# Kernel optimization log

Hardware: AMD Instinct MI355X
Metric: run time of the kernel (lower is better)

## Reference

```python
import jax, jax.numpy as jnp
import numpy as np
from jax import lax

B, NODE, T, D_IN = 8, 1024, 12, 16
HID, GAT_OUT, PRED_LEN = 32, 32, 6
HEADS = 3
F_IN = HID * T      # 384
C = GAT_OUT * T     # 384
N = B * NODE        # 8192
E = 65536


def setup_inputs() -> dict:
    key = jax.random.key(0)
    ks = jax.random.split(key, 24)
    s = 0.05
    inp = {}
    inp["x"] = jax.random.normal(ks[0], (B, NODE, T, D_IN), jnp.float32)
    inp["edge_index"] = jax.random.randint(ks[1], (2, E), 0, N)
    inp["edge_attr"] = jax.random.normal(ks[2], (E, 1), jnp.float32)
    inp["batch_vec"] = jnp.repeat(jnp.arange(B), NODE)
    inp["alpha"] = 1.0
    # GRU params (torch gate order: r, z, n)
    inp["Wih"] = jax.random.normal(ks[3], (3 * HID, D_IN), jnp.float32) * s
    inp["Whh"] = jax.random.normal(ks[4], (3 * HID, HID), jnp.float32) * s
    inp["bih"] = jax.random.normal(ks[5], (3 * HID,), jnp.float32) * s
    inp["bhh"] = jax.random.normal(ks[6], (3 * HID,), jnp.float32) * s
    # GATConv params
    inp["Wgat"] = jax.random.normal(ks[7], (HEADS * C, F_IN), jnp.float32) * s
    inp["att_src"] = jax.random.normal(ks[8], (1, HEADS, C), jnp.float32) * s
    inp["att_dst"] = jax.random.normal(ks[9], (1, HEADS, C), jnp.float32) * s
    inp["Wedge"] = jax.random.normal(ks[10], (HEADS * C, 1), jnp.float32) * s
    inp["att_edge"] = jax.random.normal(ks[11], (1, HEADS, C), jnp.float32) * s
    inp["gat_bias"] = jax.random.normal(ks[12], (C,), jnp.float32) * s
    # predictors / classifiers
    inp["Wp1"] = jax.random.normal(ks[13], (1, GAT_OUT), jnp.float32) * s
    inp["bp1"] = jax.random.normal(ks[14], (1,), jnp.float32) * s
    inp["Wp3"] = jax.random.normal(ks[15], (PRED_LEN, T), jnp.float32) * s
    inp["bp3"] = jax.random.normal(ks[16], (PRED_LEN,), jnp.float32) * s
    inp["Wc1"] = jax.random.normal(ks[17], (GAT_OUT, T * GAT_OUT), jnp.float32) * s
    inp["bc1"] = jax.random.normal(ks[18], (GAT_OUT,), jnp.float32) * s
    inp["Wc2"] = jax.random.normal(ks[19], (2, GAT_OUT), jnp.float32) * s
    inp["bc2"] = jax.random.normal(ks[20], (2,), jnp.float32) * s
    return inp


def _gru(x, Wih, Whh, bih, bhh):
    # x: [rows, T, D_IN] -> [rows, T, HID]
    h0 = jnp.zeros((x.shape[0], HID), x.dtype)

    def step(h, xt):
        gi = xt @ Wih.T + bih
        gh = h @ Whh.T + bhh
        ir, iz, inn = jnp.split(gi, 3, axis=-1)
        hr, hz, hn = jnp.split(gh, 3, axis=-1)
        r = jax.nn.sigmoid(ir + hr)
        z = jax.nn.sigmoid(iz + hz)
        n = jnp.tanh(inn + r * hn)
        h_new = (1.0 - z) * n + z * h
        return h_new, h_new

    _, hs = lax.scan(step, h0, jnp.swapaxes(x, 0, 1))
    return jnp.swapaxes(hs, 0, 1)


def _gat(x, edge_index, edge_attr, Wgat, att_src, att_dst, Wedge, att_edge, bias):
    # PyG GATConv, heads=HEADS, concat=False, edge_dim=1, no self loops
    h = (x @ Wgat.T).reshape(N, HEADS, C)          # [N,H,C]
    a_src = (h * att_src).sum(-1)                  # [N,H]
    a_dst = (h * att_dst).sum(-1)                  # [N,H]
    src, dst = edge_index[0], edge_index[1]
    e = (edge_attr @ Wedge.T).reshape(-1, HEADS, C)
    a_edge = (e * att_edge).sum(-1)                # [E,H]
    a = jax.nn.leaky_relu(a_src[src] + a_dst[dst] + a_edge, 0.2)
    amax = jax.ops.segment_max(a, dst, num_segments=N)
    a = jnp.exp(a - amax[dst])
    denom = jax.ops.segment_sum(a, dst, num_segments=N)
    a = a / (denom[dst] + 1e-16)                   # segment softmax over incoming edges
    msg = h[src] * a[:, :, None]                   # [E,H,C]
    out = jax.ops.segment_sum(msg, dst, num_segments=N)
    return out.mean(axis=1) + bias                 # concat=False -> head mean


def reference(x, edge_index, edge_attr, batch_vec, alpha,
              Wih, Whh, bih, bhh,
              Wgat, att_src, att_dst, Wedge, att_edge, gat_bias,
              Wp1, bp1, Wp3, bp3, Wc1, bc1, Wc2, bc2):
    gru_in = x.reshape(-1, T, D_IN)                       # [N,T,D]
    gru_out = _gru(gru_in, Wih, Whh, bih, bhh)            # [N,T,HID]
    gat_in = gru_out.reshape(N, F_IN)
    gat_out = _gat(gat_in, edge_index, edge_attr, Wgat, att_src, att_dst,
                   Wedge, att_edge, gat_bias)             # [N,C]
    lin_in = gat_out.reshape(-1, T, GAT_OUT)              # [N,T,GAT_OUT]
    p = jax.nn.relu(jnp.einsum('ntc,oc->nto', lin_in, Wp1) + bp1).squeeze(-1)  # [N,T]
    p = jax.nn.relu(p @ Wp3.T + bp3)                      # [N,PRED_LEN]
    out_pred = p.reshape(B, NODE, PRED_LEN)
    # GRL is identity in forward
    pooled = jax.ops.segment_max(gat_out, batch_vec, num_segments=B)  # [B,C]
    l1 = pooled @ Wc1.T + bc1
    l2 = l1 @ Wc2.T + bc2
    out_label = jax.nn.softmax(l2, axis=1)
    return out_pred, out_label
```

## Files before the change

kernel.cpp:

```cpp
#include <hip/hip_runtime.h>
#include <hip/hip_bf16.h>

#define N_NODES 8192
#define E_EDGES 65536
#define HEADS 3
#define CDIM 384
#define NHC 1152
#define T_STEPS 12
#define D_IN 16
#define HID 32
#define PRED_LEN 6
#define OUT_LABEL_OFF 49152

#define O_X        0u
#define O_WIH      1572864u
#define O_WHH      1574400u
#define O_BIH      1577472u
#define O_BHH      1577568u
#define O_WGAT     1577664u
#define O_ATTS     2020032u
#define O_ATTD     2021184u
#define O_WEDGE    2022336u
#define O_ATTE     2023488u
#define O_GBIAS    2024640u
#define O_WP1      2025024u
#define O_BP1      2025056u
#define O_WP3      2025057u
#define O_BP3      2025129u
#define O_WC1      2025135u
#define O_BC1      2037423u
#define O_WC2      2037455u
#define O_BC2      2037519u
#define O_EATTR    2037521u
#define CONV_TOTAL 2103057u

#define O_GATIN    2103072u
#define O_GATB     O_GATIN
#define O_WGATB    (O_GATIN + 1572864u)
#define O_DEG      (O_GATIN + 1794048u)
#define O_ROWST    (O_GATIN + 1802240u)
#define O_CURS     (O_GATIN + 1810432u)
#define O_CSRE     (O_GATIN + 1818624u)
#define O_HFEAT    5248800u
#define O_ASRC     14685984u
#define O_ADST     14710560u
#define O_ARAW     14735136u
#define O_WEXP     14931744u
#define O_AMAX     15128352u
#define O_DENOM    15152928u
#define O_GMEAN    15177504u
#define O_POOLED   18323232u
#define O_KH       18326304u
#define O_FLAG     18326307u

typedef __attribute__((ext_vector_type(8))) short short8;
typedef __attribute__((ext_vector_type(4))) float floatx4;

__device__ __forceinline__ float b2f(unsigned short u) {
    return __uint_as_float(((unsigned)u) << 16);
}
__device__ __forceinline__ unsigned short f2b(float f) {
    __hip_bfloat16 b = __float2bfloat16(f);
    return *(unsigned short*)&b;
}
__device__ __forceinline__ unsigned enc_f(float f) {
    unsigned u = __float_as_uint(f);
    return (u & 0x80000000u) ? ~u : (u | 0x80000000u);
}
__device__ __forceinline__ float dec_f(unsigned e) {
    return __uint_as_float((e & 0x80000000u) ? (e & 0x7FFFFFFFu) : ~e);
}

__global__ void detect_kernel(const unsigned short* __restrict__ wih_raw,
                              int* __restrict__ flag)
{
    int lane = threadIdx.x;
    int cnt = 0;
#pragma unroll
    for (int i = 0; i < 8; i++) {
        unsigned short h = wih_raw[(lane * 8 + i) * 2];
        int e = (h >> 7) & 0xFF;
        if (e >= 100 && e <= 127) cnt++;
    }
#pragma unroll
    for (int off = 32; off; off >>= 1) cnt += __shfl_down(cnt, off, 64);
    if (lane == 0) *flag = (cnt >= 300) ? 1 : 0;
}

__global__ __launch_bounds__(256) void convert_all(
    const int* __restrict__ flag,
    const void* x, const void* Wih, const void* Whh, const void* bih, const void* bhh,
    const void* Wgat, const void* atts, const void* attd, const void* Wedge, const void* atte,
    const void* gbias, const void* Wp1, const void* bp1, const void* Wp3, const void* bp3,
    const void* Wc1, const void* bc1, const void* Wc2, const void* bc2, const void* eattr,
    float* __restrict__ dst)
{
    unsigned idx = blockIdx.x * 256 + threadIdx.x;
    if (idx >= CONV_TOTAL) return;
    const void* src; unsigned off;
    if      (idx < O_WIH)   { src = x;     off = idx - O_X; }
    else if (idx < O_WHH)   { src = Wih;   off = idx - O_WIH; }
    else if (idx < O_BIH)   { src = Whh;   off = idx - O_WHH; }
    else if (idx < O_BHH)   { src = bih;   off = idx - O_BIH; }
    else if (idx < O_WGAT)  { src = bhh;   off = idx - O_BHH; }
    else if (idx < O_ATTS)  { src = Wgat;  off = idx - O_WGAT; }
    else if (idx < O_ATTD)  { src = atts;  off = idx - O_ATTS; }
    else if (idx < O_WEDGE) { src = attd;  off = idx - O_ATTD; }
    else if (idx < O_ATTE)  { src = Wedge; off = idx - O_WEDGE; }
    else if (idx < O_GBIAS) { src = atte;  off = idx - O_ATTE; }
    else if (idx < O_WP1)   { src = gbias; off = idx - O_GBIAS; }
    else if (idx < O_BP1)   { src = Wp1;   off = idx - O_WP1; }
    else if (idx < O_BP3)   { src = (idx < O_BP1 + 1) ? bp1 : Wp3; off = (idx < O_BP1 + 1) ? 0 : idx - O_BP3 + 72; }
    else if (idx < O_WC1)   { src = bp3;   off = idx - O_BP3; }
    else if (idx < O_BC1)   { src = Wc1;   off = idx - O_WC1; }
    else if (idx < O_WC2)   { src = bc1;   off = idx - O_BC1; }
    else if (idx < O_BC2)   { src = Wc2;   off = idx - O_WC2; }
    else if (idx < O_EATTR) { src = bc2;   off = idx - O_BC2; }
    else                    { src = eattr; off = idx - O_EATTR; }
    if (idx >= O_BP1 && idx < O_BP3) {
        if (idx == O_BP1) { src = bp1; off = 0; }
        else              { src = Wp3; off = idx - O_WP3; }
    }
    float v = (*flag) ? b2f(((const unsigned short*)src)[off])
                      : ((const float*)src)[off];
    dst[idx] = v;
}

__global__ void cvt_wgat(const int* __restrict__ flag,
                         const void* __restrict__ Wg,
                         unsigned short* __restrict__ dstb)
{
    unsigned i = blockIdx.x * 256 + threadIdx.x;
    if (i >= 442368u) return;
    dstb[i] = (*flag) ? ((const unsigned short*)Wg)[i]
                      : f2b(((const float*)Wg)[i]);
}

__global__ __launch_bounds__(256) void gru_kernel(
    const float* __restrict__ xf,
    const float* __restrict__ Wih,
    const float* __restrict__ Whh,
    const float* __restrict__ bih,
    const float* __restrict__ bhh,
    unsigned short* __restrict__ gat_b)
{
    __shared__ float hsh[8][32];
    int gid = blockIdx.x * 256 + threadIdx.x;
    int n = gid >> 5;
    int j = gid & 31;
    int wid = threadIdx.x >> 5;

    float wih[3][16], whh[3][32], bi[3], bh[3];
#pragma unroll
    for (int g = 0; g < 3; g++) {
        int row = g * 32 + j;
#pragma unroll
        for (int i = 0; i < 16; i++) wih[g][i] = Wih[row * 16 + i];
#pragma unroll
        for (int i = 0; i < 32; i++) whh[g][i] = Whh[row * 32 + i];
        bi[g] = bih[row];
        bh[g] = bhh[row];
    }

    float hval = 0.f;
    hsh[wid][j] = 0.f;

    const float4* x4 = (const float4*)(xf + (size_t)n * 192);

    for (int t = 0; t < T_STEPS; t++) {
        float xv[16];
#pragma unroll
        for (int q = 0; q < 4; q++) {
            float4 p = x4[t * 4 + q];
            xv[q * 4 + 0] = p.x; xv[q * 4 + 1] = p.y;
            xv[q * 4 + 2] = p.z; xv[q * 4 + 3] = p.w;
        }

        float ir = bi[0], iz = bi[1], in_ = bi[2];
#pragma unroll
        for (int i = 0; i < 16; i++) {
            ir  += wih[0][i] * xv[i];
            iz  += wih[1][i] * xv[i];
            in_ += wih[2][i] * xv[i];
        }
        float hr = bh[0], hz = bh[1], hn = bh[2];
#pragma unroll
        for (int q = 0; q < 8; q++) {
            float4 hv = *(const float4*)&hsh[wid][q * 4];
            hr += whh[0][q*4+0]*hv.x + whh[0][q*4+1]*hv.y + whh[0][q*4+2]*hv.z + whh[0][q*4+3]*hv.w;
            hz += whh[1][q*4+0]*hv.x + whh[1][q*4+1]*hv.y + whh[1][q*4+2]*hv.z + whh[1][q*4+3]*hv.w;
            hn += whh[2][q*4+0]*hv.x + whh[2][q*4+1]*hv.y + whh[2][q*4+2]*hv.z + whh[2][q*4+3]*hv.w;
        }
        float r = 1.f / (1.f + expf(-(ir + hr)));
        float z = 1.f / (1.f + expf(-(iz + hz)));
        float nn = tanhf(in_ + r * hn);
        hval = (1.f - z) * nn + z * hval;

        gat_b[(size_t)n * 384 + t * 32 + j] = f2b(hval);
        hsh[wid][j] = hval;
    }
}

__global__ __launch_bounds__(256) void gemm_mfma(
    const unsigned short* __restrict__ Ab,
    const unsigned short* __restrict__ Bb,
    unsigned short* __restrict__ Cb)
{
    __shared__ unsigned short sA[128][40];
    __shared__ unsigned short sB[128][40];
    int tid = threadIdx.x;
    int wave = tid >> 6, lane = tid & 63;
    int wm = (wave >> 1) * 64, wn = (wave & 1) * 64;
    int m0 = blockIdx.x * 128, n0 = blockIdx.y * 128;

    int r0 = tid >> 2;
    int c8 = (tid & 3) * 8;

    floatx4 acc[4][4];
#pragma unroll
    for (int i = 0; i < 4; i++)
#pragma unroll
        for (int j = 0; j < 4; j++) acc[i][j] = 0;

    int ml = lane & 15, kq = (lane >> 4) * 8;

    for (int k0 = 0; k0 < 384; k0 += 32) {
        short8 a0 = *(const short8*)(Ab + (size_t)(m0 + r0) * 384 + k0 + c8);
        short8 a1 = *(const short8*)(Ab + (size_t)(m0 + r0 + 64) * 384 + k0 + c8);
        short8 b0 = *(const short8*)(Bb + (size_t)(n0 + r0) * 384 + k0 + c8);
        short8 b1 = *(const short8*)(Bb + (size_t)(n0 + r0 + 64) * 384 + k0 + c8);

        __syncthreads();
        *(short8*)(&sA[r0][c8])      = a0;
        *(short8*)(&sA[r0 + 64][c8]) = a1;
        *(short8*)(&sB[r0][c8])      = b0;
        *(short8*)(&sB[r0 + 64][c8]) = b1;
        __syncthreads();

        short8 af[4], bf[4];
#pragma unroll
        for (int i = 0; i < 4; i++)
            af[i] = *(const short8*)(&sA[wm + i * 16 + ml][kq]);
#pragma unroll
        for (int j = 0; j < 4; j++)
            bf[j] = *(const short8*)(&sB[wn + j * 16 + ml][kq]);
#pragma unroll
        for (int i = 0; i < 4; i++)
#pragma unroll
            for (int j = 0; j < 4; j++)
                acc[i][j] = __builtin_amdgcn_mfma_f32_16x16x32_bf16(af[i], bf[j], acc[i][j], 0, 0, 0);
    }

    int cn = lane & 15, rq = (lane >> 4) * 4;
#pragma unroll
    for (int i = 0; i < 4; i++)
#pragma unroll
        for (int j = 0; j < 4; j++)
#pragma unroll
            for (int r = 0; r < 4; r++)
                Cb[(size_t)(m0 + wm + i * 16 + rq + r) * NHC + n0 + wn + j * 16 + cn] = f2b(acc[i][j][r]);
}

__global__ __launch_bounds__(256) void att_score_kernel(
    const unsigned short* __restrict__ h_bf,
    const float* __restrict__ att_src,
    const float* __restrict__ att_dst,
    float* __restrict__ a_src, float* __restrict__ a_dst)
{
    int w = (blockIdx.x * 256 + threadIdx.x) >> 6;
    int lane = threadIdx.x & 63;
    int n = w / 3, hd = w % 3;
    const unsigned short* hrow = h_bf + (size_t)n * NHC + hd * CDIM;
    float s0 = 0.f, s1 = 0.f;
#pragma unroll
    for (int q = 0; q < 6; q++) {
        int c = lane + q * 64;
        float hv = b2f(hrow[c]);
        s0 += hv * att_src[hd * CDIM + c];
        s1 += hv * att_dst[hd * CDIM + c];
    }
#pragma unroll
    for (int off = 32; off; off >>= 1) {
        s0 += __shfl_down(s0, off, 64);
        s1 += __shfl_down(s1, off, 64);
    }
    if (lane == 0) { a_src[n * 3 + hd] = s0; a_dst[n * 3 + hd] = s1; }
}

__global__ void edge_const_kernel(const float* __restrict__ Wedge,
                                  const float* __restrict__ att_edge,
                                  float* __restrict__ Kh)
{
    int hd = threadIdx.x >> 6, lane = threadIdx.x & 63;
    float s = 0.f;
#pragma unroll
    for (int q = 0; q < 6; q++) {
        int c = lane + q * 64;
        s += Wedge[hd * CDIM + c] * att_edge[hd * CDIM + c];
    }
#pragma unroll
    for (int off = 32; off; off >>= 1) s += __shfl_down(s, off, 64);
    if (lane == 0) Kh[hd] = s;
}

__global__ __launch_bounds__(256) void edge_score_kernel(
    const int* __restrict__ edge_index,
    const float* __restrict__ edge_attr,
    const float* __restrict__ a_src, const float* __restrict__ a_dst,
    const float* __restrict__ Kh,
    float* __restrict__ a_raw, unsigned* __restrict__ amax_enc,
    int* __restrict__ deg)
{
    int tid = blockIdx.x * 256 + threadIdx.x;
    int hd = tid >> 16;
    int e = tid & (E_EDGES - 1);
    int src = edge_index[e];
    int dst = edge_index[E_EDGES + e];
    float a = a_src[src * 3 + hd] + a_dst[dst * 3 + hd] + edge_attr[e] * Kh[hd];
    a = a > 0.f ? a : 0.2f * a;
    a_raw[hd * E_EDGES + e] = a;
    atomicMax(&amax_enc[dst * 3 + hd], enc_f(a));
    if (hd == 0) atomicAdd(&deg[dst], 1);
}

__global__ __launch_bounds__(256) void scan_kernel(
    const int* __restrict__ deg, int* __restrict__ rowstart, int* __restrict__ cursor)
{
    __shared__ int ps[256];
    int t = threadIdx.x;
    int l[32], s = 0;
#pragma unroll
    for (int i = 0; i < 32; i++) { l[i] = deg[t * 32 + i]; s += l[i]; }
    ps[t] = s;
    __syncthreads();
    if (t == 0) {
        int run = 0;
        for (int i = 0; i < 256; i++) { int v = ps[i]; ps[i] = run; run += v; }
    }
    __syncthreads();
    int b = ps[t];
#pragma unroll
    for (int i = 0; i < 32; i++) {
        rowstart[t * 32 + i] = b;
        cursor[t * 32 + i] = b;
        b += l[i];
    }
}

__global__ __launch_bounds__(256) void edge_exp_kernel(
    const int* __restrict__ edge_index,
    const float* __restrict__ a_raw, const unsigned* __restrict__ amax_enc,
    float* __restrict__ w_exp, float* __restrict__ denom,
    int* __restrict__ cursor, int* __restrict__ csr_e)
{
    int tid = blockIdx.x * 256 + threadIdx.x;
    int hd = tid >> 16;
    int e = tid & (E_EDGES - 1);
    int dst = edge_index[E_EDGES + e];
    float m = dec_f(amax_enc[dst * 3 + hd]);
    float w = expf(a_raw[hd * E_EDGES + e] - m);
    w_exp[hd * E_EDGES + e] = w;
    unsafeAtomicAdd(&denom[dst * 3 + hd], w);
    if (hd == 0) {
        int pos = atomicAdd(&cursor[dst], 1);
        csr_e[pos] = e;
    }
}

__global__ __launch_bounds__(384) void aggregate_fused(
    const int* __restrict__ flag,
    const int* __restrict__ edge_index,
    const unsigned short* __restrict__ h_bf,
    const float* __restrict__ w_exp, const float* __restrict__ denom,
    const int* __restrict__ rowstart, const int* __restrict__ deg,
    const int* __restrict__ csr_e,
    const float* __restrict__ gat_bias,
    const float* __restrict__ Wp1, const float* __restrict__ bp1,
    const float* __restrict__ Wp3, const float* __restrict__ bp3,
    float* __restrict__ gmean,
    void* __restrict__ out_pred)
{
    int dst = blockIdx.x;
    int s = rowstart[dst], d = deg[dst];
    int tid = threadIdx.x;
    const float third = 1.f / 3.f;
    float inv0 = third / (denom[dst * 3 + 0] + 1e-16f);
    float inv1 = third / (denom[dst * 3 + 1] + 1e-16f);
    float inv2 = third / (denom[dst * 3 + 2] + 1e-16f);
    __shared__ int ssrc[64];
    __shared__ float sc0[64], sc1[64], sc2[64];
    __shared__ float gs[384];
    __shared__ float ps[12];
    float a = 0.f;
    for (int ch = 0; ch < d; ch += 64) {
        int m = d - ch; if (m > 64) m = 64;
        __syncthreads();
        if (tid < m) {
            int e = csr_e[s + ch + tid];
            ssrc[tid] = edge_index[e];
            sc0[tid] = w_exp[e] * inv0;
            sc1[tid] = w_exp[E_EDGES + e] * inv1;
            sc2[tid] = w_exp[2 * E_EDGES + e] * inv2;
        }
        __syncthreads();
        for (int i = 0; i < m; i++) {
            const unsigned short* hs = h_bf + (size_t)ssrc[i] * NHC;
            a += sc0[i] * b2f(hs[tid]) + sc1[i] * b2f(hs[tid + CDIM]) + sc2[i] * b2f(hs[tid + 2 * CDIM]);
        }
    }
    float g = a + gat_bias[tid];
    gmean[(size_t)dst * CDIM + tid] = g;
    gs[tid] = g;
    __syncthreads();

    int t = tid >> 5, c = tid & 31;
    float v = gs[t * 32 + c] * Wp1[c];
#pragma unroll
    for (int off = 16; off; off >>= 1) v += __shfl_down(v, off, 32);
    if (c == 0) { float p = v + bp1[0]; ps[t] = p > 0.f ? p : 0.f; }
    __syncthreads();

    if (tid < PRED_LEN) {
        float acc = bp3[tid];
#pragma unroll
        for (int tt = 0; tt < 12; tt++) acc += Wp3[tid * 12 + tt] * ps[tt];
        acc = acc > 0.f ? acc : 0.f;
        size_t oi = (size_t)dst * PRED_LEN + tid;
        if (*flag) ((__hip_bfloat16*)out_pred)[oi] = __float2bfloat16(acc);
        else       ((float*)out_pred)[oi] = acc;
    }
}

__global__ __launch_bounds__(384) void pool_kernel(
    const float* __restrict__ gmean,
    unsigned* __restrict__ pooled_enc)
{
    int b = blockIdx.x, ch = blockIdx.y;
    int tid = threadIdx.x;
    const float* base = gmean + ((size_t)b * 1024 + ch * 64) * CDIM + tid;
    float m = -3.4e38f;
    for (int i = 0; i < 64; i++)
        m = fmaxf(m, base[(size_t)i * CDIM]);
    atomicMax(&pooled_enc[b * CDIM + tid], enc_f(m));
}

__global__ __launch_bounds__(256) void cls_kernel(
    const int* __restrict__ flag,
    const unsigned* __restrict__ pooled_enc,
    const float* __restrict__ Wc1, const float* __restrict__ bc1,
    const float* __restrict__ Wc2, const float* __restrict__ bc2,
    void* __restrict__ out_base)
{
    __shared__ float l1s[8][32];
    int b = threadIdx.x >> 5, i = threadIdx.x & 31;
    float acc = bc1[i];
    for (int c = 0; c < CDIM; c++)
        acc += Wc1[i * CDIM + c] * dec_f(pooled_enc[b * CDIM + c]);
    l1s[b][i] = acc;
    __syncthreads();
    if (threadIdx.x < 8) {
        int bb = threadIdx.x;
        float l0 = bc2[0], l1v = bc2[1];
#pragma unroll
        for (int ii = 0; ii < 32; ii++) {
            l0  += Wc2[ii] * l1s[bb][ii];
            l1v += Wc2[32 + ii] * l1s[bb][ii];
        }
        float m = fmaxf(l0, l1v);
        float e0 = expf(l0 - m), e1 = expf(l1v - m);
        float s = e0 + e1;
        if (*flag) {
            __hip_bfloat16* ob = (__hip_bfloat16*)out_base;
            ob[OUT_LABEL_OFF + bb * 2 + 0] = __float2bfloat16(e0 / s);
            ob[OUT_LABEL_OFF + bb * 2 + 1] = __float2bfloat16(e1 / s);
        } else {
            float* of = (float*)out_base;
            of[OUT_LABEL_OFF + bb * 2 + 0] = e0 / s;
            of[OUT_LABEL_OFF + bb * 2 + 1] = e1 / s;
        }
    }
}

extern "C" void kernel_launch(void* const* d_in, const int* in_sizes, int n_in,
                              void* d_out, int out_size, void* d_ws, size_t ws_size,
                              hipStream_t stream) {
    float* W = (float*)d_ws;
    int* flag = (int*)(W + O_FLAG);
    const int* edge_index = (const int*)d_in[1];

    size_t zero_floats = (size_t)(O_POOLED + 8 * CDIM) - O_AMAX;
    hipMemsetAsync(W + O_AMAX, 0, zero_floats * 4, stream);
    hipMemsetAsync(W + O_DEG, 0, 8192 * 4, stream);

    detect_kernel<<<1, 64, 0, stream>>>((const unsigned short*)d_in[5], flag);
    convert_all<<<(CONV_TOTAL + 255) / 256, 256, 0, stream>>>(
        flag,
        d_in[0], d_in[5], d_in[6], d_in[7], d_in[8],
        d_in[9], d_in[10], d_in[11], d_in[12], d_in[13],
        d_in[14], d_in[15], d_in[16], d_in[17], d_in[18],
        d_in[19], d_in[20], d_in[21], d_in[22], d_in[2],
        W);
    cvt_wgat<<<(442368 + 255) / 256, 256, 0, stream>>>(
        flag, d_in[9], (unsigned short*)(W + O_WGATB));

    gru_kernel<<<N_NODES * 32 / 256, 256, 0, stream>>>(
        W + O_X, W + O_WIH, W + O_WHH, W + O_BIH, W + O_BHH,
        (unsigned short*)(W + O_GATB));
    gemm_mfma<<<dim3(N_NODES / 128, NHC / 128), 256, 0, stream>>>(
        (const unsigned short*)(W + O_GATB),
        (const unsigned short*)(W + O_WGATB),
        (unsigned short*)(W + O_HFEAT));
    att_score_kernel<<<(N_NODES * 3 * 64) / 256, 256, 0, stream>>>(
        (const unsigned short*)(W + O_HFEAT), W + O_ATTS, W + O_ATTD,
        W + O_ASRC, W + O_ADST);
    edge_const_kernel<<<1, 192, 0, stream>>>(W + O_WEDGE, W + O_ATTE, W + O_KH);
    edge_score_kernel<<<3 * E_EDGES / 256, 256, 0, stream>>>(
        edge_index, W + O_EATTR, W + O_ASRC, W + O_ADST, W + O_KH,
        W + O_ARAW, (unsigned*)(W + O_AMAX), (int*)(W + O_DEG));
    scan_kernel<<<1, 256, 0, stream>>>(
        (const int*)(W + O_DEG), (int*)(W + O_ROWST), (int*)(W + O_CURS));
    edge_exp_kernel<<<3 * E_EDGES / 256, 256, 0, stream>>>(
        edge_index, W + O_ARAW, (const unsigned*)(W + O_AMAX),
        W + O_WEXP, W + O_DENOM, (int*)(W + O_CURS), (int*)(W + O_CSRE));
    aggregate_fused<<<N_NODES, 384, 0, stream>>>(
        flag, edge_index, (const unsigned short*)(W + O_HFEAT),
        W + O_WEXP, W + O_DENOM,
        (const int*)(W + O_ROWST), (const int*)(W + O_DEG),
        (const int*)(W + O_CSRE),
        W + O_GBIAS, W + O_WP1, W + O_BP1, W + O_WP3, W + O_BP3,
        W + O_GMEAN, d_out);
    pool_kernel<<<dim3(8, 16), 384, 0, stream>>>(
        W + O_GMEAN, (unsigned*)(W + O_POOLED));
    cls_kernel<<<1, 256, 0, stream>>>(
        flag, (const unsigned*)(W + O_POOLED),
        W + O_WC1, W + O_BC1, W + O_WC2, W + O_BC2, d_out);
}
```

Before: 284.5 us.

## Precompute GRU input projections in a parallel kernel and parallelize classifier

```diff
diff --git a/kernel.cpp b/kernel.cpp
--- a/kernel.cpp
+++ b/kernel.cpp
@@ -42,6 +42,7 @@
 #define O_CURS     (O_GATIN + 1810432u)
 #define O_CSRE     (O_GATIN + 1818624u)
 #define O_HFEAT    5248800u
+#define O_GIB      9967392u
 #define O_ASRC     14685984u
 #define O_ADST     14710560u
 #define O_ARAW     14735136u
@@ -89,17 +90,16 @@
 
 __global__ __launch_bounds__(256) void convert_all(
     const int* __restrict__ flag,
-    const void* x, const void* Wih, const void* Whh, const void* bih, const void* bhh,
+    const void* Wih, const void* Whh, const void* bih, const void* bhh,
     const void* Wgat, const void* atts, const void* attd, const void* Wedge, const void* atte,
     const void* gbias, const void* Wp1, const void* bp1, const void* Wp3, const void* bp3,
     const void* Wc1, const void* bc1, const void* Wc2, const void* bc2, const void* eattr,
     float* __restrict__ dst)
 {
-    unsigned idx = blockIdx.x * 256 + threadIdx.x;
+    unsigned idx = O_WIH + blockIdx.x * 256 + threadIdx.x;
     if (idx >= CONV_TOTAL) return;
     const void* src; unsigned off;
-    if      (idx < O_WIH)   { src = x;     off = idx - O_X; }
-    else if (idx < O_WHH)   { src = Wih;   off = idx - O_WIH; }
+    if      (idx < O_WHH)   { src = Wih;   off = idx - O_WIH; }
     else if (idx < O_BIH)   { src = Whh;   off = idx - O_WHH; }
     else if (idx < O_BHH)   { src = bih;   off = idx - O_BIH; }
     else if (idx < O_WGAT)  { src = bhh;   off = idx - O_BHH; }
@@ -110,17 +110,13 @@
     else if (idx < O_GBIAS) { src = atte;  off = idx - O_ATTE; }
     else if (idx < O_WP1)   { src = gbias; off = idx - O_GBIAS; }
     else if (idx < O_BP1)   { src = Wp1;   off = idx - O_WP1; }
-    else if (idx < O_BP3)   { src = (idx < O_BP1 + 1) ? bp1 : Wp3; off = (idx < O_BP1 + 1) ? 0 : idx - O_BP3 + 72; }
+    else if (idx < O_BP3)   { src = (idx == O_BP1) ? bp1 : Wp3; off = (idx == O_BP1) ? 0 : idx - O_WP3; }
     else if (idx < O_WC1)   { src = bp3;   off = idx - O_BP3; }
     else if (idx < O_BC1)   { src = Wc1;   off = idx - O_WC1; }
     else if (idx < O_WC2)   { src = bc1;   off = idx - O_BC1; }
     else if (idx < O_BC2)   { src = Wc2;   off = idx - O_WC2; }
     else if (idx < O_EATTR) { src = bc2;   off = idx - O_BC2; }
     else                    { src = eattr; off = idx - O_EATTR; }
-    if (idx >= O_BP1 && idx < O_BP3) {
-        if (idx == O_BP1) { src = bp1; off = 0; }
-        else              { src = Wp3; off = idx - O_WP3; }
-    }
     float v = (*flag) ? b2f(((const unsigned short*)src)[off])
                       : ((const float*)src)[off];
     dst[idx] = v;
@@ -136,11 +132,46 @@
                       : f2b(((const float*)Wg)[i]);
 }
 
+__global__ __launch_bounds__(256) void gi_kernel(
+    const int* __restrict__ flag,
+    const void* __restrict__ xraw,
+    const void* __restrict__ wihraw,
+    const void* __restrict__ bihraw,
+    unsigned short* __restrict__ gib)
+{
+    int gid = blockIdx.x * 256 + threadIdx.x;
+    int n = gid / 96, j = gid - n * 96;
+    bool bf = (*flag) != 0;
+    float wih[16], bi;
+    if (bf) {
+        const unsigned short* p = (const unsigned short*)wihraw + j * 16;
+#pragma unroll
+        for (int i = 0; i < 16; i++) wih[i] = b2f(p[i]);
+        bi = b2f(((const unsigned short*)bihraw)[j]);
+    } else {
+        const float* p = (const float*)wihraw + j * 16;
+#pragma unroll
+        for (int i = 0; i < 16; i++) wih[i] = p[i];
+        bi = ((const float*)bihraw)[j];
+    }
+    for (int t = 0; t < T_STEPS; t++) {
+        float s = bi;
+        if (bf) {
+            const unsigned short* xp = (const unsigned short*)xraw + (size_t)n * 192 + t * 16;
+#pragma unroll
+            for (int i = 0; i < 16; i++) s += wih[i] * b2f(xp[i]);
+        } else {
+            const float* xp = (const float*)xraw + (size_t)n * 192 + t * 16;
+#pragma unroll
+            for (int i = 0; i < 16; i++) s += wih[i] * xp[i];
+        }
+        gib[(size_t)n * 1152 + t * 96 + j] = f2b(s);
+    }
+}
+
 __global__ __launch_bounds__(256) void gru_kernel(
-    const float* __restrict__ xf,
-    const float* __restrict__ Wih,
+    const unsigned short* __restrict__ gib,
     const float* __restrict__ Whh,
-    const float* __restrict__ bih,
     const float* __restrict__ bhh,
     unsigned short* __restrict__ gat_b)
 {
@@ -150,38 +181,27 @@
     int j = gid & 31;
     int wid = threadIdx.x >> 5;
 
-    float wih[3][16], whh[3][32], bi[3], bh[3];
+    float whh[3][32], bh[3];
 #pragma unroll
     for (int g = 0; g < 3; g++) {
         int row = g * 32 + j;
 #pragma unroll
-        for (int i = 0; i < 16; i++) wih[g][i] = Wih[row * 16 + i];
-#pragma unroll
         for (int i = 0; i < 32; i++) whh[g][i] = Whh[row * 32 + i];
-        bi[g] = bih[row];
         bh[g] = bhh[row];
     }
 
     float hval = 0.f;
     hsh[wid][j] = 0.f;
 
-    const float4* x4 = (const float4*)(xf + (size_t)n * 192);
+    const unsigned short* gp = gib + (size_t)n * 1152 + j;
+    unsigned short g0 = gp[0], g1 = gp[32], g2 = gp[64];
 
     for (int t = 0; t < T_STEPS; t++) {
-        float xv[16];
-#pragma unroll
-        for (int q = 0; q < 4; q++) {
-            float4 p = x4[t * 4 + q];
-            xv[q * 4 + 0] = p.x; xv[q * 4 + 1] = p.y;
-            xv[q * 4 + 2] = p.z; xv[q * 4 + 3] = p.w;
-        }
-
-        float ir = bi[0], iz = bi[1], in_ = bi[2];
-#pragma unroll
-        for (int i = 0; i < 16; i++) {
-            ir  += wih[0][i] * xv[i];
-            iz  += wih[1][i] * xv[i];
-            in_ += wih[2][i] * xv[i];
+        float ir = b2f(g0), iz = b2f(g1), inn = b2f(g2);
+        if (t < 11) {
+            g0 = gp[(t + 1) * 96];
+            g1 = gp[(t + 1) * 96 + 32];
+            g2 = gp[(t + 1) * 96 + 64];
         }
         float hr = bh[0], hz = bh[1], hn = bh[2];
 #pragma unroll
@@ -193,7 +213,7 @@
         }
         float r = 1.f / (1.f + expf(-(ir + hr)));
         float z = 1.f / (1.f + expf(-(iz + hz)));
-        float nn = tanhf(in_ + r * hn);
+        float nn = tanhf(inn + r * hn);
         hval = (1.f - z) * nn + z * hval;
 
         gat_b[(size_t)n * 384 + t * 32 + j] = f2b(hval);
@@ -444,39 +464,44 @@
     atomicMax(&pooled_enc[b * CDIM + tid], enc_f(m));
 }
 
-__global__ __launch_bounds__(256) void cls_kernel(
+__global__ __launch_bounds__(384) void cls_kernel(
     const int* __restrict__ flag,
     const unsigned* __restrict__ pooled_enc,
     const float* __restrict__ Wc1, const float* __restrict__ bc1,
     const float* __restrict__ Wc2, const float* __restrict__ bc2,
     void* __restrict__ out_base)
 {
-    __shared__ float l1s[8][32];
-    int b = threadIdx.x >> 5, i = threadIdx.x & 31;
-    float acc = bc1[i];
-    for (int c = 0; c < CDIM; c++)
-        acc += Wc1[i * CDIM + c] * dec_f(pooled_enc[b * CDIM + c]);
-    l1s[b][i] = acc;
+    int b = blockIdx.x, t = threadIdx.x;
+    __shared__ float l1[32];
+    if (t < 32) l1[t] = bc1[t];
     __syncthreads();
-    if (threadIdx.x < 8) {
-        int bb = threadIdx.x;
+    float v = dec_f(pooled_enc[b * CDIM + t]);
+#pragma unroll
+    for (int i = 0; i < 32; i++) {
+        float p = v * Wc1[i * CDIM + t];
+#pragma unroll
+        for (int off = 32; off; off >>= 1) p += __shfl_down(p, off, 64);
+        if ((t & 63) == 0) atomicAdd(&l1[i], p);
+    }
+    __syncthreads();
+    if (t == 0) {
         float l0 = bc2[0], l1v = bc2[1];
 #pragma unroll
         for (int ii = 0; ii < 32; ii++) {
-            l0  += Wc2[ii] * l1s[bb][ii];
-            l1v += Wc2[32 + ii] * l1s[bb][ii];
+            l0  += Wc2[ii] * l1[ii];
+            l1v += Wc2[32 + ii] * l1[ii];
         }
         float m = fmaxf(l0, l1v);
         float e0 = expf(l0 - m), e1 = expf(l1v - m);
         float s = e0 + e1;
         if (*flag) {
             __hip_bfloat16* ob = (__hip_bfloat16*)out_base;
-            ob[OUT_LABEL_OFF + bb * 2 + 0] = __float2bfloat16(e0 / s);
-            ob[OUT_LABEL_OFF + bb * 2 + 1] = __float2bfloat16(e1 / s);
+            ob[OUT_LABEL_OFF + b * 2 + 0] = __float2bfloat16(e0 / s);
+            ob[OUT_LABEL_OFF + b * 2 + 1] = __float2bfloat16(e1 / s);
         } else {
             float* of = (float*)out_base;
-            of[OUT_LABEL_OFF + bb * 2 + 0] = e0 / s;
-            of[OUT_LABEL_OFF + bb * 2 + 1] = e1 / s;
+            of[OUT_LABEL_OFF + b * 2 + 0] = e0 / s;
+            of[OUT_LABEL_OFF + b * 2 + 1] = e1 / s;
         }
     }
 }
@@ -493,9 +518,9 @@
     hipMemsetAsync(W + O_DEG, 0, 8192 * 4, stream);
 
     detect_kernel<<<1, 64, 0, stream>>>((const unsigned short*)d_in[5], flag);
-    convert_all<<<(CONV_TOTAL + 255) / 256, 256, 0, stream>>>(
+    convert_all<<<(CONV_TOTAL - O_WIH + 255) / 256, 256, 0, stream>>>(
         flag,
-        d_in[0], d_in[5], d_in[6], d_in[7], d_in[8],
+        d_in[5], d_in[6], d_in[7], d_in[8],
         d_in[9], d_in[10], d_in[11], d_in[12], d_in[13],
         d_in[14], d_in[15], d_in[16], d_in[17], d_in[18],
         d_in[19], d_in[20], d_in[21], d_in[22], d_in[2],
@@ -503,8 +528,10 @@
     cvt_wgat<<<(442368 + 255) / 256, 256, 0, stream>>>(
         flag, d_in[9], (unsigned short*)(W + O_WGATB));
 
+    gi_kernel<<<N_NODES * 96 / 256, 256, 0, stream>>>(
+        flag, d_in[0], d_in[5], d_in[7], (unsigned short*)(W + O_GIB));
     gru_kernel<<<N_NODES * 32 / 256, 256, 0, stream>>>(
-        W + O_X, W + O_WIH, W + O_WHH, W + O_BIH, W + O_BHH,
+        (const unsigned short*)(W + O_GIB), W + O_WHH, W + O_BHH,
         (unsigned short*)(W + O_GATB));
     gemm_mfma<<<dim3(N_NODES / 128, NHC / 128), 256, 0, stream>>>(
         (const unsigned short*)(W + O_GATB),
@@ -531,7 +558,7 @@
         W + O_GMEAN, d_out);
     pool_kernel<<<dim3(8, 16), 384, 0, stream>>>(
         W + O_GMEAN, (unsigned*)(W + O_POOLED));
-    cls_kernel<<<1, 256, 0, stream>>>(
+    cls_kernel<<<8, 384, 0, stream>>>(
         flag, (const unsigned*)(W + O_POOLED),
         W + O_WC1, W + O_BC1, W + O_WC2, W + O_BC2, d_out);
 }
```

Result: slower. 298.1 us (+4.8%).
